# Kernel tuning notes

Hardware: AMD Instinct MI355X
Metric: run time of the kernel (lower is better)

Reference implementation:

```python
import jax, jax.numpy as jnp
import numpy as np

N_NODES = 100000
N_EDGES = 800000
N_GRAPHS = 512
D_IN = 128
D_H = 128
N_LAYERS = 3
EPS = 1e-5


def setup_inputs() -> dict:
    key = jax.random.key(0)
    ks = jax.random.split(key, 8)
    x = jax.random.normal(ks[0], (N_NODES, D_IN), dtype=jnp.float32)
    edge_index = jax.random.randint(ks[1], (2, N_EDGES), 0, N_NODES, dtype=jnp.int64)
    batch = jnp.sort(jax.random.randint(ks[2], (N_NODES,), 0, N_GRAPHS, dtype=jnp.int64))
    s = 1.0 / np.sqrt(D_H)
    Ws = jax.random.normal(ks[3], (N_LAYERS, D_H, D_H), dtype=jnp.float32) * s
    bs = jnp.zeros((N_LAYERS, D_H), dtype=jnp.float32)
    gammas = jnp.ones((N_LAYERS, D_H), dtype=jnp.float32)
    betas = jnp.zeros((N_LAYERS, D_H), dtype=jnp.float32)
    W1 = jax.random.normal(ks[4], (D_H, D_H), dtype=jnp.float32) * s
    b1 = jnp.zeros((D_H,), dtype=jnp.float32)
    W2 = jax.random.normal(ks[5], (D_H, 1), dtype=jnp.float32) * s
    b2 = jnp.zeros((1,), dtype=jnp.float32)
    return {"x": x, "edge_index": edge_index, "batch": batch, "Ws": Ws, "bs": bs,
            "gammas": gammas, "betas": betas, "W1": W1, "b1": b1, "W2": W2, "b2": b2}


def reference(x, edge_index, batch, Ws, bs, gammas, betas, W1, b1, W2, b2):
    N = x.shape[0]
    src, dst = edge_index[0], edge_index[1]
    # GCN symmetric norm with self-loops: deg = in-degree + 1 (self loop weight 1)
    deg = jax.ops.segment_sum(jnp.ones_like(dst, dtype=jnp.float32), dst, num_segments=N) + 1.0
    dinv = jax.lax.rsqrt(deg)                      # [N]
    enorm = (dinv[src] * dinv[dst])[:, None]       # [E,1]
    self_w = (1.0 / deg)[:, None]                  # [N,1] self-loop norm dinv_i^2

    h = x
    for l in range(N_LAYERS):
        h = h @ Ws[l]                                                    # linear first (as PyG GCNConv)
        h = jax.ops.segment_sum(enorm * h[src], dst, num_segments=N) + h * self_w
        h = h + bs[l]
        # BatchNorm1d, training-mode per-feature stats (biased variance)
        mu = jnp.mean(h, axis=0)
        var = jnp.mean(jnp.square(h - mu), axis=0)
        h = (h - mu) * jax.lax.rsqrt(var + EPS) * gammas[l] + betas[l]
        h = jax.nn.relu(h)                                               # dropout p=0 -> identity

    # global mean pool over subgraphs
    sums = jax.ops.segment_sum(h, batch, num_segments=N_GRAPHS)
    cnt = jax.ops.segment_sum(jnp.ones((N,), jnp.float32), batch, num_segments=N_GRAPHS)
    Z = sums / jnp.maximum(cnt, 1.0)[:, None]

    # MLP head
    hz = jax.nn.relu(Z @ W1 + b1)
    logits = hz @ W2 + b2                           # [N_GRAPHS, 1]
    return logits
```

## Files before the change

### kernel.cpp

```cpp
#include <hip/hip_runtime.h>
#include <hip/hip_bf16.h>
#include <hip/hip_fp16.h>

#define N_NODES 100000
#define N_EDGES 800000
#define N_GRAPHS 512
#define D 128
#define EPSV 1e-5f

#define NBLK 256
#define EPB  3125
#define NBUK 391
#define MAXB 3072

#define LSTR 68
#define WOFF 4352

#define NSLOT 64

typedef _Float16 half8 __attribute__((ext_vector_type(8)));
typedef float floatx16 __attribute__((ext_vector_type(16)));

__device__ __forceinline__ float relu_f(float x){ return fmaxf(x, 0.0f); }

__device__ __forceinline__ void scan512(int* sd, int t)
{
    for (int off = 1; off < 512; off <<= 1){
        int i2 = t + 256;
        int v1 = (t  >= off) ? sd[t  - off] : 0;
        int v2 = (i2 >= off) ? sd[i2 - off] : 0;
        __syncthreads();
        sd[t]  += v1;
        sd[i2] += v2;
        __syncthreads();
    }
}

__global__ __launch_bounds__(256) void k_front(const int* __restrict__ dst,
                                               int* __restrict__ blockHist,
                                               const float* __restrict__ Ws,
                                               unsigned int* __restrict__ wpack,
                                               unsigned int* __restrict__ zbase,
                                               int zn,
                                               const int* __restrict__ batch,
                                               int* __restrict__ gstart,
                                               int* __restrict__ row_ptr)
{
    __shared__ int h[NBUK];
    int j = blockIdx.x, t = threadIdx.x;
    if (j < NBLK){
        for (int u = t; u < NBUK; u += 256) h[u] = 0;
        __syncthreads();
        int e0 = j * EPB;
        for (int e = e0 + t; e < e0 + EPB; e += 256)
            atomicAdd(&h[dst[e] >> 8], 1);
        __syncthreads();
        for (int u = t; u < NBUK; u += 256) blockHist[j * NBUK + u] = h[u];
    } else {
        int b = j - NBLK;
        int idx = b * 256 + t;
        if (idx == 0){
            row_ptr[N_NODES] = N_EDGES;
            gstart[N_GRAPHS] = N_NODES;
        }
        if (idx < 3 * 128 * 64){
            int l  = idx >> 13;
            int r  = idx & 8191;
            int c  = r >> 6;
            int k2 = r & 63;
            const float* W = Ws + l * D * D;
            __half2 hh = __floats2half2_rn(W[(size_t)(2 * k2) * D + c],
                                           W[(size_t)(2 * k2 + 1) * D + c]);
            wpack[idx] = *(unsigned int*)&hh;
        }
        int stride = 96 * 256;
        for (int i = idx; i < zn; i += stride) zbase[i] = 0u;
        if (idx < N_GRAPHS){
            int g = idx;
            int lo = 0, hi = N_NODES;
            while (lo < hi){ int m = (lo + hi) >> 1; if (batch[m] < g) lo = m + 1; else hi = m; }
            gstart[g] = lo;
        }
    }
}

__global__ __launch_bounds__(256) void k_p2a(const int* __restrict__ blockHist,
                                             int* __restrict__ colScan,
                                             int* __restrict__ bucketTotal)
{
    __shared__ int sd[256];
    int b = blockIdx.x, t = threadIdx.x;
    int v = blockHist[t * NBUK + b];
    sd[t] = v;
    __syncthreads();
    for (int off = 1; off < 256; off <<= 1){
        int u = (t >= off) ? sd[t - off] : 0;
        __syncthreads();
        sd[t] += u;
        __syncthreads();
    }
    colScan[t * NBUK + b] = sd[t] - v;
    if (t == 255) bucketTotal[b] = sd[255];
}

__global__ __launch_bounds__(256) void k_p3(const int* __restrict__ src,
                                            const int* __restrict__ dst,
                                            const int* __restrict__ colScan,
                                            const int* __restrict__ bucketTotal,
                                            int2* __restrict__ ebuf)
{
    __shared__ int sd[512];
    __shared__ int cur[NBUK];
    int j = blockIdx.x, t = threadIdx.x;
    int i2 = t + 256;
    sd[t]  = (t  < NBUK) ? bucketTotal[t]  : 0;
    sd[i2] = (i2 < NBUK) ? bucketTotal[i2] : 0;
    __syncthreads();
    scan512(sd, t);
    if (t < NBUK)
        cur[t]  = (sd[t]  - bucketTotal[t])  + colScan[j * NBUK + t];
    if (i2 < NBUK)
        cur[i2] = (sd[i2] - bucketTotal[i2]) + colScan[j * NBUK + i2];
    __syncthreads();
    int e0 = j * EPB;
    for (int e = e0 + t; e < e0 + EPB; e += 256){
        int s = src[e], d = dst[e];
        int pos = atomicAdd(&cur[d >> 8], 1);
        int2 v; v.x = s; v.y = d;
        ebuf[pos] = v;
    }
}

__global__ __launch_bounds__(256) void k_p4(const int2* __restrict__ ebuf,
                                            const int* __restrict__ bucketTotal,
                                            int* __restrict__ row_ptr,
                                            int* __restrict__ csr_src,
                                            float* __restrict__ dinv)
{
    __shared__ int2 stash[MAXB];
    __shared__ int sdScan[512];
    __shared__ int bins[256];
    __shared__ int sd[256];
    int b = blockIdx.x, t = threadIdx.x;
    int i2 = t + 256;
    sdScan[t]  = (t  < NBUK) ? bucketTotal[t]  : 0;
    sdScan[i2] = (i2 < NBUK) ? bucketTotal[i2] : 0;
    __syncthreads();
    scan512(sdScan, t);
    int cntb = bucketTotal[b];
    int base = sdScan[b] - cntb;
    bool st = (cntb <= MAXB);
    bins[t] = 0;
    __syncthreads();
    for (int i = t; i < cntb; i += 256){
        int2 ed = ebuf[base + i];
        if (st) stash[i] = ed;
        atomicAdd(&bins[ed.y & 255], 1);
    }
    __syncthreads();
    int a0 = bins[t];
    sd[t] = a0;
    __syncthreads();
    for (int off = 1; off < 256; off <<= 1){
        int v = (t >= off) ? sd[t - off] : 0;
        __syncthreads();
        sd[t] += v;
        __syncthreads();
    }
    int pex = sd[t] - a0;
    int node = b * 256 + t;
    if (node < N_NODES){
        row_ptr[node] = base + pex;
        float d = (float)(a0 + 1);
        dinv[node]  = rsqrtf(d);
    }
    __syncthreads();
    bins[t] = pex;
    __syncthreads();
    for (int i = t; i < cntb; i += 256){
        int2 ed = st ? stash[i] : ebuf[base + i];
        int pos = atomicAdd(&bins[ed.y & 255], 1);
        csr_src[base + pos] = ed.x;
    }
}

__global__ __launch_bounds__(256) void k_gemm(const void* __restrict__ Ain,
                                              const unsigned int* __restrict__ wp,
                                              const float* __restrict__ Spart,
                                              const float* __restrict__ Qpart,
                                              const float* __restrict__ gamma,
                                              const float* __restrict__ beta,
                                              const float* __restrict__ dinv,
                                              __half* __restrict__ outh,
                                              int mode)
{
    __shared__ unsigned int lds32[WOFF + 128 * LSTR];
    __shared__ float sscale[128];
    __shared__ float sshift[128];
    int tid = threadIdx.x;
    int rowBase = blockIdx.x * 64;

    if (mode){
        float* red = (float*)lds32;
        int f = tid & 127;
        const float* sp = (tid < 128) ? Spart : Qpart;
        float acc = 0.f;
        #pragma unroll 16
        for (int s = 0; s < NSLOT; s++)
            acc += sp[s * 128 + f];
        red[tid] = acc;
        __syncthreads();
        if (tid < 128){
            float Sv = red[f];
            float Qv = red[f + 128];
            float mean = Sv * (1.0f / N_NODES);
            float var  = fmaxf(Qv * (1.0f / N_NODES) - mean * mean, 0.0f);
            float inv  = rsqrtf(var + EPSV);
            float gm = gamma[f] * inv;
            sscale[f] = gm;
            sshift[f] = beta[f] - mean * gm;
        }
        __syncthreads();
    }

    if (mode == 0){
        const float* A = (const float*)Ain;
        #pragma unroll
        for (int rep = 0; rep < 8; rep++){
            int f  = rep * 256 + tid;
            int m  = f >> 5;
            int c4 = f & 31;
            int row = rowBase + m;
            if (row >= N_NODES) row = N_NODES - 1;
            float4 v = *(const float4*)(A + (size_t)row * D + c4 * 4);
            __half2 h0 = __floats2half2_rn(v.x, v.y);
            __half2 h1 = __floats2half2_rn(v.z, v.w);
            uint2 u; u.x = *(unsigned int*)&h0; u.y = *(unsigned int*)&h1;
            *(uint2*)&lds32[m * LSTR + 2 * c4] = u;
        }
    } else {
        const __half* A16 = (const __half*)Ain;
        #pragma unroll
        for (int rep = 0; rep < 4; rep++){
            int f  = rep * 256 + tid;
            int m  = f >> 4;
            int c8 = f & 15;
            int row = rowBase + m;
            if (row >= N_NODES) row = N_NODES - 1;
            uint4 v = *(const uint4*)(A16 + (size_t)row * D + c8 * 8);
            float4 sc0 = *(const float4*)&sscale[c8 * 8];
            float4 sc1 = *(const float4*)&sscale[c8 * 8 + 4];
            float4 sh0 = *(const float4*)&sshift[c8 * 8];
            float4 sh1 = *(const float4*)&sshift[c8 * 8 + 4];
            float2 f0 = __half22float2(*(__half2*)&v.x);
            float2 f1 = __half22float2(*(__half2*)&v.y);
            float2 f2 = __half22float2(*(__half2*)&v.z);
            float2 f3 = __half22float2(*(__half2*)&v.w);
            f0.x = relu_f(fmaf(f0.x, sc0.x, sh0.x));
            f0.y = relu_f(fmaf(f0.y, sc0.y, sh0.y));
            f1.x = relu_f(fmaf(f1.x, sc0.z, sh0.z));
            f1.y = relu_f(fmaf(f1.y, sc0.w, sh0.w));
            f2.x = relu_f(fmaf(f2.x, sc1.x, sh1.x));
            f2.y = relu_f(fmaf(f2.y, sc1.y, sh1.y));
            f3.x = relu_f(fmaf(f3.x, sc1.z, sh1.z));
            f3.y = relu_f(fmaf(f3.y, sc1.w, sh1.w));
            __half2 h0 = __floats2half2_rn(f0.x, f0.y);
            __half2 h1 = __floats2half2_rn(f1.x, f1.y);
            __half2 h2 = __floats2half2_rn(f2.x, f2.y);
            __half2 h3 = __floats2half2_rn(f3.x, f3.y);
            uint4 u;
            u.x = *(unsigned int*)&h0; u.y = *(unsigned int*)&h1;
            u.z = *(unsigned int*)&h2; u.w = *(unsigned int*)&h3;
            *(uint4*)&lds32[m * LSTR + 4 * c8] = u;
        }
    }
    {
        const uint4* gw = (const uint4*)wp;
        #pragma unroll
        for (int rep = 0; rep < 8; rep++){
            int f = rep * 256 + tid;
            int c = f >> 4;
            int q = f & 15;
            uint4 v = gw[f];
            *(uint4*)&lds32[WOFF + c * LSTR + 4 * q] = v;
        }
    }
    __syncthreads();

    int lane = tid & 63, wv = tid >> 6;
    int quad = lane >> 5;
    int ml   = (lane & 31) + (wv & 1) * 32;
    int cA   = (wv >> 1) * 64;
    int c0   = cA + (lane & 31);
    int c1   = c0 + 32;
    const unsigned int* aRow  = lds32 + ml * LSTR;
    const unsigned int* bRow0 = lds32 + WOFF + c0 * LSTR;
    const unsigned int* bRow1 = lds32 + WOFF + c1 * LSTR;
    floatx16 acc0 = {};
    floatx16 acc1 = {};
    #pragma unroll
    for (int ch = 0; ch < 8; ch++){
        int o = ch * 8 + quad * 4;
        half8 af = *(const half8*)(aRow  + o);
        half8 b0 = *(const half8*)(bRow0 + o);
        half8 b1 = *(const half8*)(bRow1 + o);
        acc0 = __builtin_amdgcn_mfma_f32_32x32x16_f16(af, b0, acc0, 0, 0, 0);
        acc1 = __builtin_amdgcn_mfma_f32_32x32x16_f16(af, b1, acc1, 0, 0, 0);
    }
    int rBase = rowBase + (wv & 1) * 32 + 4 * quad;
    #pragma unroll
    for (int r = 0; r < 16; r++){
        int outRow = rBase + (r & 3) + 8 * (r >> 2);
        if (outRow < N_NODES){
            float dv = dinv[outRow];
            outh[(size_t)outRow * D + c0] = __float2half(acc0[r] * dv);
            outh[(size_t)outRow * D + c1] = __float2half(acc1[r] * dv);
        }
    }
}

__device__ __forceinline__ void accum8(float* acc, uint4 v)
{
    float2 f0 = __half22float2(*(__half2*)&v.x);
    float2 f1 = __half22float2(*(__half2*)&v.y);
    float2 f2 = __half22float2(*(__half2*)&v.z);
    float2 f3 = __half22float2(*(__half2*)&v.w);
    acc[0] += f0.x; acc[1] += f0.y; acc[2] += f1.x; acc[3] += f1.y;
    acc[4] += f2.x; acc[5] += f2.y; acc[6] += f3.x; acc[7] += f3.y;
}

__global__ __launch_bounds__(256) void k_agg(const __half* __restrict__ t,
                                             const int* __restrict__ row_ptr,
                                             const int* __restrict__ csr_src,
                                             const float* __restrict__ dinv,
                                             const float* __restrict__ bias,
                                             __half* __restrict__ outb,
                                             float* __restrict__ Spart,
                                             float* __restrict__ Qpart)
{
    __shared__ float ldsS[4][128];
    __shared__ float ldsQ[4][128];
    int tid  = threadIdx.x;
    int lane = tid & 63;
    int wv   = tid >> 6;
    int q    = lane & 15;
    int g    = lane >> 4;
    const uint4* t4 = (const uint4*)t;
    uint4* out4 = (uint4*)outb;

    float4 bia = ((const float4*)bias)[2 * q];
    float4 bib = ((const float4*)bias)[2 * q + 1];

    float sa[8] = {0.f,0.f,0.f,0.f,0.f,0.f,0.f,0.f};
    float qa[8] = {0.f,0.f,0.f,0.f,0.f,0.f,0.f,0.f};

    int i0 = blockIdx.x * 32 + wv * 8 + g * 2;

    for (int n = 0; n < 2; n++){
        int i  = i0 + n;
        int p  = row_ptr[i];
        int pe = row_ptr[i + 1];
        float acc[8];
        {
            uint4 v = t4[(size_t)i * 16 + q];
            float2 f0 = __half22float2(*(__half2*)&v.x);
            float2 f1 = __half22float2(*(__half2*)&v.y);
            float2 f2 = __half22float2(*(__half2*)&v.z);
            float2 f3 = __half22float2(*(__half2*)&v.w);
            acc[0] = f0.x; acc[1] = f0.y; acc[2] = f1.x; acc[3] = f1.y;
            acc[4] = f2.x; acc[5] = f2.y; acc[6] = f3.x; acc[7] = f3.y;
        }
        for (; p + 4 <= pe; p += 4){
            int s0 = csr_src[p],     s1 = csr_src[p + 1];
            int s2 = csr_src[p + 2], s3 = csr_src[p + 3];
            uint4 v0 = t4[(size_t)s0 * 16 + q];
            uint4 v1 = t4[(size_t)s1 * 16 + q];
            uint4 v2 = t4[(size_t)s2 * 16 + q];
            uint4 v3 = t4[(size_t)s3 * 16 + q];
            accum8(acc, v0); accum8(acc, v1); accum8(acc, v2); accum8(acc, v3);
        }
        for (; p < pe; ++p){
            int s = csr_src[p];
            uint4 v = t4[(size_t)s * 16 + q];
            accum8(acc, v);
        }
        float dvi = dinv[i];
        acc[0] = fmaf(acc[0], dvi, bia.x);
        acc[1] = fmaf(acc[1], dvi, bia.y);
        acc[2] = fmaf(acc[2], dvi, bia.z);
        acc[3] = fmaf(acc[3], dvi, bia.w);
        acc[4] = fmaf(acc[4], dvi, bib.x);
        acc[5] = fmaf(acc[5], dvi, bib.y);
        acc[6] = fmaf(acc[6], dvi, bib.z);
        acc[7] = fmaf(acc[7], dvi, bib.w);
        __half2 o0 = __floats2half2_rn(acc[0], acc[1]);
        __half2 o1 = __floats2half2_rn(acc[2], acc[3]);
        __half2 o2 = __floats2half2_rn(acc[4], acc[5]);
        __half2 o3 = __floats2half2_rn(acc[6], acc[7]);
        uint4 ov;
        ov.x = *(unsigned int*)&o0; ov.y = *(unsigned int*)&o1;
        ov.z = *(unsigned int*)&o2; ov.w = *(unsigned int*)&o3;
        out4[(size_t)i * 16 + q] = ov;
        #pragma unroll
        for (int k = 0; k < 8; k++){
            sa[k] += acc[k];
            qa[k]  = fmaf(acc[k], acc[k], qa[k]);
        }
    }

    #pragma unroll
    for (int k = 0; k < 8; k++){
        sa[k] += __shfl_xor(sa[k], 16);
        sa[k] += __shfl_xor(sa[k], 32);
        qa[k] += __shfl_xor(qa[k], 16);
        qa[k] += __shfl_xor(qa[k], 32);
    }
    if (g == 0){
        #pragma unroll
        for (int k = 0; k < 8; k++){
            ldsS[wv][8 * q + k] = sa[k];
            ldsQ[wv][8 * q + k] = qa[k];
        }
    }
    __syncthreads();
    int slotBase = (blockIdx.x & (NSLOT - 1)) * 128;
    if (tid < 128){
        float s = ldsS[0][tid] + ldsS[1][tid] + ldsS[2][tid] + ldsS[3][tid];
        atomicAdd(&Spart[slotBase + tid], s);
    } else {
        int f = tid - 128;
        float qv = ldsQ[0][f] + ldsQ[1][f] + ldsQ[2][f] + ldsQ[3][f];
        atomicAdd(&Qpart[slotBase + f], qv);
    }
}

__global__ __launch_bounds__(256) void k_tail(const __half* __restrict__ h,
                                              const int* __restrict__ gstart,
                                              const float* __restrict__ Spart,
                                              const float* __restrict__ Qpart,
                                              const float* __restrict__ gamma,
                                              const float* __restrict__ beta,
                                              const float* __restrict__ W1,
                                              const float* __restrict__ b1,
                                              const float* __restrict__ W2,
                                              const float* __restrict__ b2,
                                              float* __restrict__ out)
{
    __shared__ float part[256];
    __shared__ float z[128];
    __shared__ float red[128];
    __shared__ float sscale[128];
    __shared__ float sshift[128];
    int g = blockIdx.x;
    int tid = threadIdx.x;
    int f = tid & 127;
    int hf = tid >> 7;

    {
        const float* sp = (tid < 128) ? Spart : Qpart;
        float acc = 0.f;
        #pragma unroll 16
        for (int s = 0; s < NSLOT; s++)
            acc += sp[s * 128 + f];
        part[tid] = acc;
        __syncthreads();
        if (tid < 128){
            float Sv = part[f];
            float Qv = part[f + 128];
            float mean = Sv * (1.0f / N_NODES);
            float var  = fmaxf(Qv * (1.0f / N_NODES) - mean * mean, 0.0f);
            float inv  = rsqrtf(var + EPSV);
            float gm = gamma[f] * inv;
            sscale[f] = gm;
            sshift[f] = beta[f] - mean * gm;
        }
        __syncthreads();
    }

    int s0 = gstart[g], s1 = gstart[g + 1];
    float scv = sscale[f], shv = sshift[f];
    float acc = 0.f;
    for (int i = s0 + hf; i < s1; i += 2)
        acc += relu_f(fmaf(__half2float(h[(size_t)i * D + f]), scv, shv));
    part[tid] = acc;
    __syncthreads();
    if (tid < 128){
        float c = fmaxf((float)(s1 - s0), 1.0f);
        z[f] = (part[f] + part[f + 128]) / c;
    }
    __syncthreads();
    float a = 0.f;
    int k0 = hf * 64;
    #pragma unroll 8
    for (int k = k0; k < k0 + 64; k++)
        a = fmaf(z[k], W1[k * D + f], a);
    part[tid] = a;
    __syncthreads();
    if (tid < 128){
        float av = relu_f(part[f] + part[f + 128] + b1[f]);
        red[f] = av * W2[f];
    }
    __syncthreads();
    for (int s2 = 64; s2 > 0; s2 >>= 1){
        if (tid < s2) red[tid] += red[tid + s2];
        __syncthreads();
    }
    if (tid == 0) out[g] = red[0] + b2[0];
}

extern "C" void kernel_launch(void* const* d_in, const int* in_sizes, int n_in,
                              void* d_out, int out_size, void* d_ws, size_t ws_size,
                              hipStream_t stream)
{
    const float* x      = (const float*)d_in[0];
    const int*   ei     = (const int*)d_in[1];
    const int*   batch  = (const int*)d_in[2];
    const float* Ws     = (const float*)d_in[3];
    const float* bs     = (const float*)d_in[4];
    const float* gammas = (const float*)d_in[5];
    const float* betas  = (const float*)d_in[6];
    const float* W1     = (const float*)d_in[7];
    const float* b1     = (const float*)d_in[8];
    const float* W2     = (const float*)d_in[9];
    const float* b2     = (const float*)d_in[10];
    float* out = (float*)d_out;

    const int* src = ei;
    const int* dst = ei + N_EDGES;

    char* w = (char*)d_ws;
    size_t off = 0;
    auto alloc = [&](size_t bytes) -> void* {
        void* p = w + off;
        off += (bytes + 255) & ~(size_t)255;
        return p;
    };
    int*   row_ptr     = (int*)  alloc((size_t)(N_NODES + 1) * 4);
    float* dinv        = (float*)alloc((size_t)N_NODES * 4);
    int*   csr_src     = (int*)  alloc((size_t)N_EDGES * 4);
    int*   blockHist   = (int*)  alloc((size_t)NBLK * NBUK * 4);
    int*   colScan     = (int*)  alloc((size_t)NBLK * NBUK * 4);
    int*   bucketTotal = (int*)  alloc((size_t)NBUK * 4);
    unsigned int* wpack = (unsigned int*)alloc((size_t)3 * 128 * 64 * 4);
    int*   gstart      = (int*)  alloc((size_t)(N_GRAPHS + 1) * 4);
    size_t zoff = off;
    float* stats       = (float*)alloc((size_t)3 * 2 * NSLOT * 128 * 4);
    size_t zend = off;
    __half* tbuf       = (__half*)alloc((size_t)N_NODES * 128 * 2);
    __half* hbuf       = (__half*)alloc((size_t)N_NODES * 128 * 2);
    if (off > ws_size) return;

    int2* ebuf = (int2*)tbuf;

    k_front<<<NBLK + 96, 256, 0, stream>>>(dst, blockHist, Ws, wpack,
                                           (unsigned int*)(w + zoff),
                                           (int)((zend - zoff) >> 2),
                                           batch, gstart, row_ptr);
    k_p2a<<<NBUK, 256, 0, stream>>>(blockHist, colScan, bucketTotal);
    k_p3 <<<NBLK, 256, 0, stream>>>(src, dst, colScan, bucketTotal, ebuf);
    k_p4 <<<NBUK, 256, 0, stream>>>(ebuf, bucketTotal, row_ptr, csr_src, dinv);

    const void* curIn = (const void*)x;
    for (int l = 0; l < 3; l++){
        float* Sp = stats + (size_t)l * 2 * NSLOT * 128;
        float* Qp = Sp + NSLOT * 128;
        float* Spm = stats + (size_t)(l - 1) * 2 * NSLOT * 128;
        float* Qpm = Spm + NSLOT * 128;
        k_gemm<<<(N_NODES + 63) / 64, 256, 0, stream>>>(
            curIn, wpack + l * 8192,
            l ? Spm : nullptr,
            l ? Qpm : nullptr,
            l ? gammas + (l - 1) * 128 : nullptr,
            l ? betas  + (l - 1) * 128 : nullptr,
            dinv, tbuf, l ? 1 : 0);
        k_agg<<<N_NODES / 32, 256, 0, stream>>>(
            tbuf, row_ptr, csr_src, dinv,
            bs + l * 128, hbuf, Sp, Qp);
        curIn = (const void*)hbuf;
    }

    {
        float* Sp2 = stats + (size_t)2 * 2 * NSLOT * 128;
        float* Qp2 = Sp2 + NSLOT * 128;
        k_tail<<<N_GRAPHS, 256, 0, stream>>>(hbuf, gstart,
                                             Sp2, Qp2,
                                             gammas + 2 * 128, betas + 2 * 128,
                                             W1, b1, W2, b2, out);
    }
}
```

Measured before the change: 346.4 us.

## Slice feature dimension into 16-wide planes for cache-resident aggregation

Stores the intermediate node features as 8 feature-sliced planes of 16 halfs each (slice-major), and changes the aggregation grid so each block handles one slice over a 512-node chunk. Each slice plane is about 3.2 MB, so the random neighbour gathers for one slice are meant to stay in L2 or LLC instead of streaming the full 25 MB array. The GEMM writes, the next GEMM's reads and the tail pooling are updated to use the new layout. In exchange, each row gather becomes a 32-byte access, CSR indices are re-read eight times, and the GEMM output stores become more scattered.

```diff
diff --git a/kernel.cpp b/kernel.cpp
--- a/kernel.cpp
+++ b/kernel.cpp
@@ -17,6 +17,10 @@
 #define WOFF 4352
 
 #define NSLOT 64
+
+#define NSLICE 8
+#define CHUNK 512
+#define NCHUNK 196
 
 typedef _Float16 half8 __attribute__((ext_vector_type(8)));
 typedef float floatx16 __attribute__((ext_vector_type(16)));
@@ -247,7 +251,8 @@
             int c8 = f & 15;
             int row = rowBase + m;
             if (row >= N_NODES) row = N_NODES - 1;
-            uint4 v = *(const uint4*)(A16 + (size_t)row * D + c8 * 8);
+            int sc = c8 >> 1, qq = c8 & 1;
+            uint4 v = *(const uint4*)(A16 + ((size_t)sc * N_NODES + row) * 16 + qq * 8);
             float4 sc0 = *(const float4*)&sscale[c8 * 8];
             float4 sc1 = *(const float4*)&sscale[c8 * 8 + 4];
             float4 sh0 = *(const float4*)&sshift[c8 * 8];
@@ -307,14 +312,16 @@
         acc0 = __builtin_amdgcn_mfma_f32_32x32x16_f16(af, b0, acc0, 0, 0, 0);
         acc1 = __builtin_amdgcn_mfma_f32_32x32x16_f16(af, b1, acc1, 0, 0, 0);
     }
+    int sc0i = c0 >> 4, w0 = c0 & 15;
+    int sc1i = c1 >> 4, w1 = c1 & 15;
     int rBase = rowBase + (wv & 1) * 32 + 4 * quad;
     #pragma unroll
     for (int r = 0; r < 16; r++){
         int outRow = rBase + (r & 3) + 8 * (r >> 2);
         if (outRow < N_NODES){
             float dv = dinv[outRow];
-            outh[(size_t)outRow * D + c0] = __float2half(acc0[r] * dv);
-            outh[(size_t)outRow * D + c1] = __float2half(acc1[r] * dv);
+            outh[((size_t)sc0i * N_NODES + outRow) * 16 + w0] = __float2half(acc0[r] * dv);
+            outh[((size_t)sc1i * N_NODES + outRow) * 16 + w1] = __float2half(acc1[r] * dv);
         }
     }
 }
@@ -338,99 +345,109 @@
                                              float* __restrict__ Spart,
                                              float* __restrict__ Qpart)
 {
-    __shared__ float ldsS[4][128];
-    __shared__ float ldsQ[4][128];
+    __shared__ float ldsS[4][16];
+    __shared__ float ldsQ[4][16];
     int tid  = threadIdx.x;
     int lane = tid & 63;
     int wv   = tid >> 6;
-    int q    = lane & 15;
-    int g    = lane >> 4;
+    int q    = lane & 1;
+    int g    = lane >> 1;
+    int s    = blockIdx.x & 7;
+    int chunk = blockIdx.x >> 3;
     const uint4* t4 = (const uint4*)t;
     uint4* out4 = (uint4*)outb;
-
-    float4 bia = ((const float4*)bias)[2 * q];
-    float4 bib = ((const float4*)bias)[2 * q + 1];
+    size_t sbase = (size_t)s * N_NODES * 2;
+
+    float4 bia = ((const float4*)bias)[s * 4 + 2 * q];
+    float4 bib = ((const float4*)bias)[s * 4 + 2 * q + 1];
 
     float sa[8] = {0.f,0.f,0.f,0.f,0.f,0.f,0.f,0.f};
     float qa[8] = {0.f,0.f,0.f,0.f,0.f,0.f,0.f,0.f};
 
-    int i0 = blockIdx.x * 32 + wv * 8 + g * 2;
-
-    for (int n = 0; n < 2; n++){
-        int i  = i0 + n;
-        int p  = row_ptr[i];
-        int pe = row_ptr[i + 1];
-        float acc[8];
-        {
-            uint4 v = t4[(size_t)i * 16 + q];
-            float2 f0 = __half22float2(*(__half2*)&v.x);
-            float2 f1 = __half22float2(*(__half2*)&v.y);
-            float2 f2 = __half22float2(*(__half2*)&v.z);
-            float2 f3 = __half22float2(*(__half2*)&v.w);
-            acc[0] = f0.x; acc[1] = f0.y; acc[2] = f1.x; acc[3] = f1.y;
-            acc[4] = f2.x; acc[5] = f2.y; acc[6] = f3.x; acc[7] = f3.y;
-        }
-        for (; p + 4 <= pe; p += 4){
-            int s0 = csr_src[p],     s1 = csr_src[p + 1];
-            int s2 = csr_src[p + 2], s3 = csr_src[p + 3];
-            uint4 v0 = t4[(size_t)s0 * 16 + q];
-            uint4 v1 = t4[(size_t)s1 * 16 + q];
-            uint4 v2 = t4[(size_t)s2 * 16 + q];
-            uint4 v3 = t4[(size_t)s3 * 16 + q];
-            accum8(acc, v0); accum8(acc, v1); accum8(acc, v2); accum8(acc, v3);
-        }
-        for (; p < pe; ++p){
-            int s = csr_src[p];
-            uint4 v = t4[(size_t)s * 16 + q];
-            accum8(acc, v);
-        }
-        float dvi = dinv[i];
-        acc[0] = fmaf(acc[0], dvi, bia.x);
-        acc[1] = fmaf(acc[1], dvi, bia.y);
-        acc[2] = fmaf(acc[2], dvi, bia.z);
-        acc[3] = fmaf(acc[3], dvi, bia.w);
-        acc[4] = fmaf(acc[4], dvi, bib.x);
-        acc[5] = fmaf(acc[5], dvi, bib.y);
-        acc[6] = fmaf(acc[6], dvi, bib.z);
-        acc[7] = fmaf(acc[7], dvi, bib.w);
-        __half2 o0 = __floats2half2_rn(acc[0], acc[1]);
-        __half2 o1 = __floats2half2_rn(acc[2], acc[3]);
-        __half2 o2 = __floats2half2_rn(acc[4], acc[5]);
-        __half2 o3 = __floats2half2_rn(acc[6], acc[7]);
-        uint4 ov;
-        ov.x = *(unsigned int*)&o0; ov.y = *(unsigned int*)&o1;
-        ov.z = *(unsigned int*)&o2; ov.w = *(unsigned int*)&o3;
-        out4[(size_t)i * 16 + q] = ov;
-        #pragma unroll
-        for (int k = 0; k < 8; k++){
-            sa[k] += acc[k];
-            qa[k]  = fmaf(acc[k], acc[k], qa[k]);
+    int i0 = chunk * CHUNK + wv * 128 + g * 4;
+
+    for (int n = 0; n < 4; n++){
+        int i = i0 + n;
+        if (i < N_NODES){
+            int p  = row_ptr[i];
+            int pe = row_ptr[i + 1];
+            float acc[8];
+            {
+                uint4 v = t4[sbase + (size_t)i * 2 + q];
+                float2 f0 = __half22float2(*(__half2*)&v.x);
+                float2 f1 = __half22float2(*(__half2*)&v.y);
+                float2 f2 = __half22float2(*(__half2*)&v.z);
+                float2 f3 = __half22float2(*(__half2*)&v.w);
+                acc[0] = f0.x; acc[1] = f0.y; acc[2] = f1.x; acc[3] = f1.y;
+                acc[4] = f2.x; acc[5] = f2.y; acc[6] = f3.x; acc[7] = f3.y;
+            }
+            for (; p + 4 <= pe; p += 4){
+                int s0 = csr_src[p],     s1 = csr_src[p + 1];
+                int s2 = csr_src[p + 2], s3 = csr_src[p + 3];
+                uint4 v0 = t4[sbase + (size_t)s0 * 2 + q];
+                uint4 v1 = t4[sbase + (size_t)s1 * 2 + q];
+                uint4 v2 = t4[sbase + (size_t)s2 * 2 + q];
+                uint4 v3 = t4[sbase + (size_t)s3 * 2 + q];
+                accum8(acc, v0); accum8(acc, v1); accum8(acc, v2); accum8(acc, v3);
+            }
+            for (; p < pe; ++p){
+                int sj = csr_src[p];
+                accum8(acc, t4[sbase + (size_t)sj * 2 + q]);
+            }
+            float dvi = dinv[i];
+            acc[0] = fmaf(acc[0], dvi, bia.x);
+            acc[1] = fmaf(acc[1], dvi, bia.y);
+            acc[2] = fmaf(acc[2], dvi, bia.z);
+            acc[3] = fmaf(acc[3], dvi, bia.w);
+            acc[4] = fmaf(acc[4], dvi, bib.x);
+            acc[5] = fmaf(acc[5], dvi, bib.y);
+            acc[6] = fmaf(acc[6], dvi, bib.z);
+            acc[7] = fmaf(acc[7], dvi, bib.w);
+            __half2 o0 = __floats2half2_rn(acc[0], acc[1]);
+            __half2 o1 = __floats2half2_rn(acc[2], acc[3]);
+            __half2 o2 = __floats2half2_rn(acc[4], acc[5]);
+            __half2 o3 = __floats2half2_rn(acc[6], acc[7]);
+            uint4 ov;
+            ov.x = *(unsigned int*)&o0; ov.y = *(unsigned int*)&o1;
+            ov.z = *(unsigned int*)&o2; ov.w = *(unsigned int*)&o3;
+            out4[sbase + (size_t)i * 2 + q] = ov;
+            #pragma unroll
+            for (int k = 0; k < 8; k++){
+                sa[k] += acc[k];
+                qa[k]  = fmaf(acc[k], acc[k], qa[k]);
+            }
         }
     }
 
     #pragma unroll
     for (int k = 0; k < 8; k++){
+        sa[k] += __shfl_xor(sa[k], 2);
+        sa[k] += __shfl_xor(sa[k], 4);
+        sa[k] += __shfl_xor(sa[k], 8);
         sa[k] += __shfl_xor(sa[k], 16);
         sa[k] += __shfl_xor(sa[k], 32);
+        qa[k] += __shfl_xor(qa[k], 2);
+        qa[k] += __shfl_xor(qa[k], 4);
+        qa[k] += __shfl_xor(qa[k], 8);
         qa[k] += __shfl_xor(qa[k], 16);
         qa[k] += __shfl_xor(qa[k], 32);
     }
     if (g == 0){
         #pragma unroll
         for (int k = 0; k < 8; k++){
-            ldsS[wv][8 * q + k] = sa[k];
-            ldsQ[wv][8 * q + k] = qa[k];
-        }
-    }
-    __syncthreads();
-    int slotBase = (blockIdx.x & (NSLOT - 1)) * 128;
-    if (tid < 128){
-        float s = ldsS[0][tid] + ldsS[1][tid] + ldsS[2][tid] + ldsS[3][tid];
-        atomicAdd(&Spart[slotBase + tid], s);
-    } else {
-        int f = tid - 128;
-        float qv = ldsQ[0][f] + ldsQ[1][f] + ldsQ[2][f] + ldsQ[3][f];
-        atomicAdd(&Qpart[slotBase + f], qv);
+            ldsS[wv][q * 8 + k] = sa[k];
+            ldsQ[wv][q * 8 + k] = qa[k];
+        }
+    }
+    __syncthreads();
+    int slot = chunk & (NSLOT - 1);
+    if (tid < 16){
+        float v = ldsS[0][tid] + ldsS[1][tid] + ldsS[2][tid] + ldsS[3][tid];
+        atomicAdd(&Spart[slot * 128 + s * 16 + tid], v);
+    } else if (tid < 32){
+        int f = tid - 16;
+        float v = ldsQ[0][f] + ldsQ[1][f] + ldsQ[2][f] + ldsQ[3][f];
+        atomicAdd(&Qpart[slot * 128 + s * 16 + f], v);
     }
 }
 
@@ -479,9 +496,10 @@
 
     int s0 = gstart[g], s1 = gstart[g + 1];
     float scv = sscale[f], shv = sshift[f];
+    const __half* hp = h + (size_t)(f >> 4) * N_NODES * 16 + (f & 15);
     float acc = 0.f;
     for (int i = s0 + hf; i < s1; i += 2)
-        acc += relu_f(fmaf(__half2float(h[(size_t)i * D + f]), scv, shv));
+        acc += relu_f(fmaf(__half2float(hp[(size_t)i * 16]), scv, shv));
     part[tid] = acc;
     __syncthreads();
     if (tid < 128){
@@ -573,7 +591,7 @@
             l ? gammas + (l - 1) * 128 : nullptr,
             l ? betas  + (l - 1) * 128 : nullptr,
             dinv, tbuf, l ? 1 : 0);
-        k_agg<<<N_NODES / 32, 256, 0, stream>>>(
+        k_agg<<<NSLICE * NCHUNK, 256, 0, stream>>>(
             tbuf, row_ptr, csr_src, dinv,
             bs + l * 128, hbuf, Sp, Qp);
         curIn = (const void*)hbuf;
```

New measurement: 499.3 us. +44.1%, slower.

## Replace bucketed two-pass CSR build with global-atomic degree count and scatter

Applied to the files above, without the earlier changes.

The CSR construction changes from a bucket histogram, column scan, bucketed edge scatter and per-bucket local sort to a direct per-node degree count with global atomics, a two-level prefix scan over nodes, and a scatter that places each edge with a global atomic cursor. This drops the intermediate int2 edge buffer and the LDS stash pass. In exchange it relies on contended global atomics over 800k edges, adds a memset launch, and makes the order of neighbours within each row nondeterministic, which can change floating-point summation order.

```diff
diff --git a/kernel.cpp b/kernel.cpp
--- a/kernel.cpp
+++ b/kernel.cpp
@@ -10,8 +10,7 @@
 
 #define NBLK 256
 #define EPB  3125
-#define NBUK 391
-#define MAXB 3072
+#define NSB  391
 
 #define LSTR 68
 #define WOFF 4352
@@ -23,21 +22,8 @@
 
 __device__ __forceinline__ float relu_f(float x){ return fmaxf(x, 0.0f); }
 
-__device__ __forceinline__ void scan512(int* sd, int t)
-{
-    for (int off = 1; off < 512; off <<= 1){
-        int i2 = t + 256;
-        int v1 = (t  >= off) ? sd[t  - off] : 0;
-        int v2 = (i2 >= off) ? sd[i2 - off] : 0;
-        __syncthreads();
-        sd[t]  += v1;
-        sd[i2] += v2;
-        __syncthreads();
-    }
-}
-
 __global__ __launch_bounds__(256) void k_front(const int* __restrict__ dst,
-                                               int* __restrict__ blockHist,
+                                               int* __restrict__ deg,
                                                const float* __restrict__ Ws,
                                                unsigned int* __restrict__ wpack,
                                                unsigned int* __restrict__ zbase,
@@ -46,16 +32,11 @@
                                                int* __restrict__ gstart,
                                                int* __restrict__ row_ptr)
 {
-    __shared__ int h[NBUK];
     int j = blockIdx.x, t = threadIdx.x;
     if (j < NBLK){
-        for (int u = t; u < NBUK; u += 256) h[u] = 0;
-        __syncthreads();
         int e0 = j * EPB;
         for (int e = e0 + t; e < e0 + EPB; e += 256)
-            atomicAdd(&h[dst[e] >> 8], 1);
-        __syncthreads();
-        for (int u = t; u < NBUK; u += 256) blockHist[j * NBUK + u] = h[u];
+            atomicAdd(&deg[dst[e]], 1);
     } else {
         int b = j - NBLK;
         int idx = b * 256 + t;
@@ -84,13 +65,14 @@
     }
 }
 
-__global__ __launch_bounds__(256) void k_p2a(const int* __restrict__ blockHist,
-                                             int* __restrict__ colScan,
-                                             int* __restrict__ bucketTotal)
+__global__ __launch_bounds__(256) void k_scanA(const int* __restrict__ deg,
+                                               int* __restrict__ cursor,
+                                               int* __restrict__ partials)
 {
     __shared__ int sd[256];
     int b = blockIdx.x, t = threadIdx.x;
-    int v = blockHist[t * NBUK + b];
+    int node = b * 256 + t;
+    int v = (node < N_NODES) ? deg[node] : 0;
     sd[t] = v;
     __syncthreads();
     for (int off = 1; off < 256; off <<= 1){
@@ -99,88 +81,51 @@
         sd[t] += u;
         __syncthreads();
     }
-    colScan[t * NBUK + b] = sd[t] - v;
-    if (t == 255) bucketTotal[b] = sd[255];
-}
-
-__global__ __launch_bounds__(256) void k_p3(const int* __restrict__ src,
-                                            const int* __restrict__ dst,
-                                            const int* __restrict__ colScan,
-                                            const int* __restrict__ bucketTotal,
-                                            int2* __restrict__ ebuf)
+    if (node < N_NODES) cursor[node] = sd[t] - v;
+    if (t == 255) partials[b] = sd[255];
+}
+
+__global__ __launch_bounds__(256) void k_scanB(const int* __restrict__ deg,
+                                               const int* __restrict__ partials,
+                                               int* __restrict__ cursor,
+                                               int* __restrict__ row_ptr,
+                                               float* __restrict__ dinv)
 {
     __shared__ int sd[512];
-    __shared__ int cur[NBUK];
+    int b = blockIdx.x, t = threadIdx.x;
+    int i2 = t + 256;
+    sd[t]  = (t  < NSB) ? partials[t]  : 0;
+    sd[i2] = (i2 < NSB) ? partials[i2] : 0;
+    __syncthreads();
+    for (int off = 1; off < 512; off <<= 1){
+        int v1 = (t  >= off) ? sd[t  - off] : 0;
+        int v2 = (i2 >= off) ? sd[i2 - off] : 0;
+        __syncthreads();
+        sd[t]  += v1;
+        sd[i2] += v2;
+        __syncthreads();
+    }
+    int base = sd[b] - partials[b];
+    int node = b * 256 + t;
+    if (node < N_NODES){
+        int rp = base + cursor[node];
+        row_ptr[node] = rp;
+        cursor[node]  = rp;
+        dinv[node]    = rsqrtf((float)(deg[node] + 1));
+    }
+}
+
+__global__ __launch_bounds__(256) void k_scatter(const int* __restrict__ src,
+                                                 const int* __restrict__ dst,
+                                                 int* __restrict__ cursor,
+                                                 int* __restrict__ csr_src)
+{
     int j = blockIdx.x, t = threadIdx.x;
-    int i2 = t + 256;
-    sd[t]  = (t  < NBUK) ? bucketTotal[t]  : 0;
-    sd[i2] = (i2 < NBUK) ? bucketTotal[i2] : 0;
-    __syncthreads();
-    scan512(sd, t);
-    if (t < NBUK)
-        cur[t]  = (sd[t]  - bucketTotal[t])  + colScan[j * NBUK + t];
-    if (i2 < NBUK)
-        cur[i2] = (sd[i2] - bucketTotal[i2]) + colScan[j * NBUK + i2];
-    __syncthreads();
     int e0 = j * EPB;
     for (int e = e0 + t; e < e0 + EPB; e += 256){
         int s = src[e], d = dst[e];
-        int pos = atomicAdd(&cur[d >> 8], 1);
-        int2 v; v.x = s; v.y = d;
-        ebuf[pos] = v;
-    }
-}
-
-__global__ __launch_bounds__(256) void k_p4(const int2* __restrict__ ebuf,
-                                            const int* __restrict__ bucketTotal,
-                                            int* __restrict__ row_ptr,
-                                            int* __restrict__ csr_src,
-                                            float* __restrict__ dinv)
-{
-    __shared__ int2 stash[MAXB];
-    __shared__ int sdScan[512];
-    __shared__ int bins[256];
-    __shared__ int sd[256];
-    int b = blockIdx.x, t = threadIdx.x;
-    int i2 = t + 256;
-    sdScan[t]  = (t  < NBUK) ? bucketTotal[t]  : 0;
-    sdScan[i2] = (i2 < NBUK) ? bucketTotal[i2] : 0;
-    __syncthreads();
-    scan512(sdScan, t);
-    int cntb = bucketTotal[b];
-    int base = sdScan[b] - cntb;
-    bool st = (cntb <= MAXB);
-    bins[t] = 0;
-    __syncthreads();
-    for (int i = t; i < cntb; i += 256){
-        int2 ed = ebuf[base + i];
-        if (st) stash[i] = ed;
-        atomicAdd(&bins[ed.y & 255], 1);
-    }
-    __syncthreads();
-    int a0 = bins[t];
-    sd[t] = a0;
-    __syncthreads();
-    for (int off = 1; off < 256; off <<= 1){
-        int v = (t >= off) ? sd[t - off] : 0;
-        __syncthreads();
-        sd[t] += v;
-        __syncthreads();
-    }
-    int pex = sd[t] - a0;
-    int node = b * 256 + t;
-    if (node < N_NODES){
-        row_ptr[node] = base + pex;
-        float d = (float)(a0 + 1);
-        dinv[node]  = rsqrtf(d);
-    }
-    __syncthreads();
-    bins[t] = pex;
-    __syncthreads();
-    for (int i = t; i < cntb; i += 256){
-        int2 ed = st ? stash[i] : ebuf[base + i];
-        int pos = atomicAdd(&bins[ed.y & 255], 1);
-        csr_src[base + pos] = ed.x;
+        int pos = atomicAdd(&cursor[d], 1);
+        csr_src[pos] = s;
     }
 }
 
@@ -538,9 +483,9 @@
     int*   row_ptr     = (int*)  alloc((size_t)(N_NODES + 1) * 4);
     float* dinv        = (float*)alloc((size_t)N_NODES * 4);
     int*   csr_src     = (int*)  alloc((size_t)N_EDGES * 4);
-    int*   blockHist   = (int*)  alloc((size_t)NBLK * NBUK * 4);
-    int*   colScan     = (int*)  alloc((size_t)NBLK * NBUK * 4);
-    int*   bucketTotal = (int*)  alloc((size_t)NBUK * 4);
+    int*   deg         = (int*)  alloc((size_t)N_NODES * 4);
+    int*   cursor      = (int*)  alloc((size_t)N_NODES * 4);
+    int*   partials    = (int*)  alloc((size_t)512 * 4);
     unsigned int* wpack = (unsigned int*)alloc((size_t)3 * 128 * 64 * 4);
     int*   gstart      = (int*)  alloc((size_t)(N_GRAPHS + 1) * 4);
     size_t zoff = off;
@@ -550,15 +495,15 @@
     __half* hbuf       = (__half*)alloc((size_t)N_NODES * 128 * 2);
     if (off > ws_size) return;
 
-    int2* ebuf = (int2*)tbuf;
-
-    k_front<<<NBLK + 96, 256, 0, stream>>>(dst, blockHist, Ws, wpack,
+    hipMemsetAsync(deg, 0, (size_t)N_NODES * 4, stream);
+
+    k_front<<<NBLK + 96, 256, 0, stream>>>(dst, deg, Ws, wpack,
                                            (unsigned int*)(w + zoff),
                                            (int)((zend - zoff) >> 2),
                                            batch, gstart, row_ptr);
-    k_p2a<<<NBUK, 256, 0, stream>>>(blockHist, colScan, bucketTotal);
-    k_p3 <<<NBLK, 256, 0, stream>>>(src, dst, colScan, bucketTotal, ebuf);
-    k_p4 <<<NBUK, 256, 0, stream>>>(ebuf, bucketTotal, row_ptr, csr_src, dinv);
+    k_scanA<<<NSB, 256, 0, stream>>>(deg, cursor, partials);
+    k_scanB<<<NSB, 256, 0, stream>>>(deg, partials, cursor, row_ptr, dinv);
+    k_scatter<<<NBLK, 256, 0, stream>>>(src, dst, cursor, csr_src);
 
     const void* curIn = (const void*)x;
     for (int l = 0; l < 3; l++){
```

New measurement: 406.8 us. +17.4%, slower.
